# Kernel optimization log

Measured on AMD Instinct MI355X. Metric: run time of the kernel, lower is better.

## Reference

```python
import jax, jax.numpy as jnp
import numpy as np

IN_DIMS = (8, 16, 8)
EMBED = 1024
HEADS = 16
HEAD_DIM = EMBED // HEADS
RANK = 16
CORE_SHAPES = [(1, 8, 8, RANK), (RANK, 16, 16, RANK), (RANK, 8, 8, 1)]


def tt_linear(x, cores, bias):
    """Apply a TT-matrix to x: [N, prod(IN_DIMS)] -> [N, prod(out_dims)].

    Cores G_k: [r_{k-1}, i_k, o_k, r_k], r_0 = r_d = 1. Sequential chain of
    small rank-bounded contractions, faithful to TTLinear.forward.
    """
    N = x.shape[0]
    t = x.reshape(N, 1, 1, -1)  # (N, O_done, r, I_rest)
    for G, i in zip(cores, IN_DIMS):
        rest = t.shape[-1] // i
        t = t.reshape(N, t.shape[1], t.shape[2], i, rest)
        # contract input mode i and left rank r -> output mode q and right rank s
        t = jnp.einsum('norik,riqs->noqsk', t, G)
        t = t.reshape(N, t.shape[1] * t.shape[2], t.shape[3], -1)
    return t.reshape(N, -1) + bias


def setup_inputs() -> dict:
    key = jax.random.key(0)
    ks = iter(jax.random.split(key, 32))
    inp = {"query": jax.random.normal(next(ks), (2, 2048, EMBED), dtype=jnp.float32)}
    for name in ("wq", "wk", "wv", "wo"):
        for ci, shp in enumerate(CORE_SHAPES):
            inp[f"{name}_c{ci}"] = jax.random.normal(next(ks), shp, dtype=jnp.float32) * 0.3
        inp[f"{name}_b"] = jax.random.normal(next(ks), (EMBED,), dtype=jnp.float32) * 0.02
    return inp


def reference(query, wq_c0, wq_c1, wq_c2, wq_b, wk_c0, wk_c1, wk_c2, wk_b,
              wv_c0, wv_c1, wv_c2, wv_b, wo_c0, wo_c1, wo_c2, wo_b):
    B, Lq, _ = query.shape
    flat = query.reshape(-1, EMBED)
    # self-attention: key = value = query
    Q = tt_linear(flat, (wq_c0, wq_c1, wq_c2), wq_b).reshape(B, Lq, HEADS, HEAD_DIM)
    K = tt_linear(flat, (wk_c0, wk_c1, wk_c2), wk_b).reshape(B, Lq, HEADS, HEAD_DIM)
    V = tt_linear(flat, (wv_c0, wv_c1, wv_c2), wv_b).reshape(B, Lq, HEADS, HEAD_DIM)
    Q = Q.transpose(0, 2, 1, 3)  # bhqd
    K = K.transpose(0, 2, 1, 3)
    V = V.transpose(0, 2, 1, 3)
    scale = HEAD_DIM ** -0.5
    scores = jnp.einsum('bhqd,bhkd->bhqk', Q, K) * scale
    attn = jax.nn.softmax(scores, axis=-1)
    ctx = jnp.einsum('bhqk,bhkd->bhqd', attn, V)
    ctx = ctx.transpose(0, 2, 1, 3).reshape(B * Lq, EMBED)
    out = tt_linear(ctx, (wo_c0, wo_c1, wo_c2), wo_b)
    return out.reshape(B, Lq, EMBED)
```

## Files before the change

kernel.cpp:

```cpp
#include <hip/hip_runtime.h>
#include <hip/hip_bf16.h>
#include <stdint.h>

#define LQ 2048
#define NTOK 4096

typedef __attribute__((ext_vector_type(8))) short short8;
typedef __attribute__((ext_vector_type(4))) float f32x4;
typedef __attribute__((ext_vector_type(16))) float f32x16;
typedef __attribute__((ext_vector_type(4))) unsigned short u16x4;

#define MFMA16(a, b, c) __builtin_amdgcn_mfma_f32_16x16x32_bf16((a), (b), (c), 0, 0, 0)
#define MFMA32(a, b, c) __builtin_amdgcn_mfma_f32_32x32x16_bf16((a), (b), (c), 0, 0, 0)

__device__ __forceinline__ unsigned short f2bf(float x) {
    union { __hip_bfloat16 b; unsigned short u; } v;
    v.b = __float2bfloat16(x);
    return v.u;
}
__device__ __forceinline__ float bf2f(unsigned short h) {
    union { uint32_t u; float f; } v; v.u = ((uint32_t)h) << 16; return v.f;
}
__device__ __forceinline__ unsigned int cvtpk_bf16(float lo, float hi_) {
    unsigned int r;
    asm("v_cvt_pk_bf16_f32 %0, %1, %2" : "=v"(r) : "v"(lo), "v"(hi_));
    return r;
}
__device__ __forceinline__ void permswap(unsigned int &a, unsigned int &b) {
    asm("v_permlane32_swap_b32 %0, %1" : "+v"(a), "+v"(b));
}

struct CorePtrs {
    const float* c0[4];
    const float* c1[4];
    const float* c2[4];
};

__global__ __launch_bounds__(256) void build_w_kernel(
    CorePtrs cp, unsigned short* __restrict__ Whi, unsigned short* __restrict__ Wlo)
{
    __shared__ float B1[16 * 16 * 16];
    const int p  = blockIdx.y;
    const int i0 = blockIdx.x >> 3;
    const int q0 = blockIdx.x & 7;
    const int t  = threadIdx.x;
    const float* __restrict__ c0 = cp.c0[p];
    const float* __restrict__ c1 = cp.c1[p];
    const float* __restrict__ c2 = cp.c2[p];

    float g0[16];
#pragma unroll
    for (int s = 0; s < 16; ++s) g0[s] = c0[(i0 * 8 + q0) * 16 + s];

    for (int idx = t; idx < 4096; idx += 256) {
        const int s2 = idx & 15;
        const int q1 = (idx >> 4) & 15;
        const int i1 = idx >> 8;
        float acc = 0.f;
#pragma unroll
        for (int s = 0; s < 16; ++s)
            acc += g0[s] * c1[((s * 16 + i1) * 16 + q1) * 16 + s2];
        B1[idx] = acc;
    }
    __syncthreads();

    const size_t base = (size_t)p * 1024 * 1024;
    for (int idx = t; idx < 16384; idx += 256) {
        const int q2 = idx & 7;
        const int i2 = (idx >> 3) & 7;
        const int q1 = (idx >> 6) & 15;
        const int i1 = idx >> 10;
        float acc = 0.f;
#pragma unroll
        for (int s2 = 0; s2 < 16; ++s2)
            acc += B1[(i1 * 16 + q1) * 16 + s2] * c2[(s2 * 8 + i2) * 8 + q2];
        const int o = q0 * 128 + q1 * 8 + q2;
        const int e = i0 * 128 + i1 * 8 + i2;
        const unsigned short hi = f2bf(acc);
        Whi[base + o * 1024 + e] = hi;
        Wlo[base + o * 1024 + e] = f2bf(acc - bf2f(hi));
    }
}

__global__ __launch_bounds__(256) void convert_x_kernel(
    const float* __restrict__ X, unsigned short* __restrict__ Xhi,
    unsigned short* __restrict__ Xlo, int n4)
{
    const int i = blockIdx.x * 256 + threadIdx.x;
    if (i >= n4) return;
    const float4 v = ((const float4*)X)[i];
    u16x4 hi, lo;
    float vv[4] = {v.x, v.y, v.z, v.w};
#pragma unroll
    for (int j = 0; j < 4; ++j) {
        unsigned short h = f2bf(vv[j]);
        hi[j] = h;
        lo[j] = f2bf(vv[j] - bf2f(h));
    }
    ((u16x4*)Xhi)[i] = hi;
    ((u16x4*)Xlo)[i] = lo;
}

template <bool SPLIT, int OUTMODE>
__global__ __launch_bounds__(256) void gemm_kernel(
    const unsigned short* __restrict__ Xh, const unsigned short* __restrict__ Xl,
    const unsigned short* __restrict__ Wh, const unsigned short* __restrict__ Wl,
    const float* __restrict__ bias, float oscale,
    unsigned short* __restrict__ Yhi, unsigned short* __restrict__ Ylo,
    float* __restrict__ Yf)
{
    __shared__ unsigned short Ah[128 * 32];
    __shared__ unsigned short Bh[128 * 32];
    __shared__ unsigned short Al[SPLIT ? 128 * 32 : 8];
    __shared__ unsigned short Bl[SPLIT ? 128 * 32 : 8];

    const int t = threadIdx.x;
    const int l = t & 63;
    const int w = t >> 6;
    const int wr = (w >> 1) * 64, wc = (w & 1) * 64;
    const int bm = blockIdx.y * 128, bn = blockIdx.x * 128;

    f32x4 acc[4][4];
#pragma unroll
    for (int i = 0; i < 4; ++i)
#pragma unroll
        for (int j = 0; j < 4; ++j) acc[i][j] = (f32x4){0.f, 0.f, 0.f, 0.f};

    const int srow = t >> 1;
    const int sch  = (t & 1) * 2;
    const int ssel = (srow >> 1) & 3;
    const int sd0  = srow * 32 + (((sch)     ^ ssel) << 3);
    const int sd1  = srow * 32 + (((sch + 1) ^ ssel) << 3);
    const size_t xoff = (size_t)(bm + srow) * 1024 + sch * 8;
    const size_t woff = (size_t)(bn + srow) * 1024 + sch * 8;

    const int fsel = ((l & 15) >> 1) & 3;
    const int fpos = ((l >> 4) ^ fsel) << 3;
    const int fra  = (wr + (l & 15)) * 32 + fpos;
    const int frb  = (wc + (l & 15)) * 32 + fpos;

    short8 pXh0, pXh1, pWh0, pWh1, pXl0, pXl1, pWl0, pWl1;
    pXh0 = *(const short8*)&Xh[xoff];     pXh1 = *(const short8*)&Xh[xoff + 8];
    pWh0 = *(const short8*)&Wh[woff];     pWh1 = *(const short8*)&Wh[woff + 8];
    if constexpr (SPLIT) {
        pXl0 = *(const short8*)&Xl[xoff]; pXl1 = *(const short8*)&Xl[xoff + 8];
        pWl0 = *(const short8*)&Wl[woff]; pWl1 = *(const short8*)&Wl[woff + 8];
    }

    for (int e0 = 0; e0 < 1024; e0 += 32) {
        __syncthreads();
        *(short8*)&Ah[sd0] = pXh0; *(short8*)&Ah[sd1] = pXh1;
        *(short8*)&Bh[sd0] = pWh0; *(short8*)&Bh[sd1] = pWh1;
        if constexpr (SPLIT) {
            *(short8*)&Al[sd0] = pXl0; *(short8*)&Al[sd1] = pXl1;
            *(short8*)&Bl[sd0] = pWl0; *(short8*)&Bl[sd1] = pWl1;
        }
        __syncthreads();

        if (e0 + 32 < 1024) {
            const size_t xo = xoff + e0 + 32, wo = woff + e0 + 32;
            pXh0 = *(const short8*)&Xh[xo];     pXh1 = *(const short8*)&Xh[xo + 8];
            pWh0 = *(const short8*)&Wh[wo];     pWh1 = *(const short8*)&Wh[wo + 8];
            if constexpr (SPLIT) {
                pXl0 = *(const short8*)&Xl[xo]; pXl1 = *(const short8*)&Xl[xo + 8];
                pWl0 = *(const short8*)&Wl[wo]; pWl1 = *(const short8*)&Wl[wo + 8];
            }
        }

        short8 af[4], bfv[4], afl[4], bfl[4];
#pragma unroll
        for (int rb = 0; rb < 4; ++rb) {
            af[rb]  = *(const short8*)&Ah[fra + rb * 512];
            bfv[rb] = *(const short8*)&Bh[frb + rb * 512];
        }
#pragma unroll
        for (int rb = 0; rb < 4; ++rb)
#pragma unroll
            for (int cb = 0; cb < 4; ++cb)
                acc[rb][cb] = MFMA16(af[rb], bfv[cb], acc[rb][cb]);
        if constexpr (SPLIT) {
#pragma unroll
            for (int rb = 0; rb < 4; ++rb) afl[rb] = *(const short8*)&Al[fra + rb * 512];
#pragma unroll
            for (int rb = 0; rb < 4; ++rb)
#pragma unroll
                for (int cb = 0; cb < 4; ++cb)
                    acc[rb][cb] = MFMA16(afl[rb], bfv[cb], acc[rb][cb]);
#pragma unroll
            for (int rb = 0; rb < 4; ++rb) bfl[rb] = *(const short8*)&Bl[frb + rb * 512];
#pragma unroll
            for (int rb = 0; rb < 4; ++rb)
#pragma unroll
                for (int cb = 0; cb < 4; ++cb)
                    acc[rb][cb] = MFMA16(af[rb], bfl[cb], acc[rb][cb]);
        }
    }

    const int r0 = (l >> 4) * 4;
    const int cc = l & 15;
#pragma unroll
    for (int rb = 0; rb < 4; ++rb)
#pragma unroll
        for (int cb = 0; cb < 4; ++cb) {
            const int col = bn + wc + cb * 16 + cc;
            const float bv = bias[col];
#pragma unroll
            for (int r = 0; r < 4; ++r) {
                const int row = bm + wr + rb * 16 + r0 + r;
                const float v = (acc[rb][cb][r] + bv) * oscale;
                if constexpr (OUTMODE == 0) {
                    const unsigned short hi = f2bf(v);
                    Yhi[(size_t)row * 1024 + col] = hi;
                    Ylo[(size_t)row * 1024 + col] = f2bf(v - bf2f(hi));
                } else if constexpr (OUTMODE == 1) {
                    Yhi[(size_t)row * 1024 + col] = f2bf(v);
                } else {
                    Yf[(size_t)row * 1024 + col] = v;
                }
            }
        }
}

__global__ __launch_bounds__(256) void transpose_kernel(
    const unsigned short* __restrict__ V, unsigned short* __restrict__ VT)
{
    __shared__ unsigned short tile[64][65];
    const int t = threadIdx.x;
    const int c0 = blockIdx.x * 64;
    const int r0 = blockIdx.y * 64;
    {
        const int r = t >> 2;
        const int q = (t & 3) * 16;
        short8 v0 = *(const short8*)&V[(size_t)(r0 + r) * 1024 + c0 + q];
        short8 v1 = *(const short8*)&V[(size_t)(r0 + r) * 1024 + c0 + q + 8];
#pragma unroll
        for (int i = 0; i < 8; ++i) {
            tile[r][q + i]     = (unsigned short)v0[i];
            tile[r][q + 8 + i] = (unsigned short)v1[i];
        }
    }
    __syncthreads();
    {
        const int c = t >> 2;
        const int g = (t & 3) * 16;
        short8 out0, out1;
#pragma unroll
        for (int i = 0; i < 8; ++i) {
            out0[i] = (short)tile[g + i][c];
            out1[i] = (short)tile[g + 8 + i][c];
        }
        *(short8*)&VT[(size_t)(c0 + c) * 4096 + r0 + g]     = out0;
        *(short8*)&VT[(size_t)(c0 + c) * 4096 + r0 + g + 8] = out1;
    }
}

__global__ __launch_bounds__(256) void attn_kernel(
    const unsigned short* __restrict__ Qh, const unsigned short* __restrict__ Ql,
    const unsigned short* __restrict__ Kh_g, const unsigned short* __restrict__ Kl_g,
    const unsigned short* __restrict__ VT, unsigned short* __restrict__ CTX)
{
    __shared__ unsigned short Khs[2][64 * 64];
    __shared__ unsigned short Kls[2][64 * 64];
    __shared__ unsigned short Vts[2][64 * 64];

    const int t = threadIdx.x;
    const int l = t & 63;
    const int w = t >> 6;
    const int qt = blockIdx.x, h = blockIdx.y, b = blockIdx.z;
    const int lq = l & 31;
    const int hi = l >> 5;
    const int tokq = b * LQ + qt * 128 + w * 32;

    short8 qhf[4], qlf[4];
    {
        const size_t qr = (size_t)(tokq + lq) * 1024 + h * 64 + hi * 8;
#pragma unroll
        for (int ds = 0; ds < 4; ++ds) {
            qhf[ds] = *(const short8*)&Qh[qr + ds * 16];
            qlf[ds] = *(const short8*)&Ql[qr + ds * 16];
        }
    }

    f32x16 o0, o1;
#pragma unroll
    for (int i = 0; i < 16; ++i) { o0[i] = 0.f; o1[i] = 0.f; }
    float m = -1e30f, lsum = 0.f;

    const int srow = t >> 2;
    const int sch  = (t & 3) * 2;
    int sdst[2];
#pragma unroll
    for (int it = 0; it < 2; ++it)
        sdst[it] = srow * 64 + (((sch + it) ^ (srow & 7)) << 3);

    short8 pf_kh[2], pf_kl[2], pf_vt[2];
    {
        const int tokk = b * LQ;
#pragma unroll
        for (int it = 0; it < 2; ++it) {
            const size_t gk = (size_t)(tokk + srow) * 1024 + h * 64 + (sch + it) * 8;
            pf_kh[it] = *(const short8*)&Kh_g[gk];
            pf_kl[it] = *(const short8*)&Kl_g[gk];
            pf_vt[it] = *(const short8*)&VT[(size_t)(h * 64 + srow) * 4096 + tokk + (sch + it) * 8];
        }
    }

    const int lq7 = lq & 7;
    int cur = 0;
    for (int kt = 0; kt < 32; ++kt) {
#pragma unroll
        for (int it = 0; it < 2; ++it) {
            *(short8*)&Khs[cur][sdst[it]] = pf_kh[it];
            *(short8*)&Kls[cur][sdst[it]] = pf_kl[it];
            *(short8*)&Vts[cur][sdst[it]] = pf_vt[it];
        }
        if (kt < 31) {
            const int tokk = b * LQ + (kt + 1) * 64;
#pragma unroll
            for (int it = 0; it < 2; ++it) {
                const size_t gk = (size_t)(tokk + srow) * 1024 + h * 64 + (sch + it) * 8;
                pf_kh[it] = *(const short8*)&Kh_g[gk];
                pf_kl[it] = *(const short8*)&Kl_g[gk];
                pf_vt[it] = *(const short8*)&VT[(size_t)(h * 64 + srow) * 4096 + tokk + (sch + it) * 8];
            }
        }
        __syncthreads();

        f32x16 s0, s1;
#pragma unroll
        for (int i = 0; i < 16; ++i) { s0[i] = 0.f; s1[i] = 0.f; }
#pragma unroll
        for (int ds = 0; ds < 4; ++ds) {
            const int slot = (((2 * ds + hi) ^ lq7) << 3);
            const int off = lq * 64 + slot;
            short8 kh0 = *(const short8*)&Khs[cur][off];
            short8 kh1 = *(const short8*)&Khs[cur][off + 2048];
            short8 kl0 = *(const short8*)&Kls[cur][off];
            short8 kl1 = *(const short8*)&Kls[cur][off + 2048];
            s0 = MFMA32(kh0, qhf[ds], s0);
            s1 = MFMA32(kh1, qhf[ds], s1);
            s0 = MFMA32(kl0, qhf[ds], s0);
            s1 = MFMA32(kl1, qhf[ds], s1);
            s0 = MFMA32(kh0, qlf[ds], s0);
            s1 = MFMA32(kh1, qlf[ds], s1);
        }

        float vm = s0[0];
#pragma unroll
        for (int i = 1; i < 16; ++i) vm = fmaxf(vm, s0[i]);
#pragma unroll
        for (int i = 0; i < 16; ++i) vm = fmaxf(vm, s1[i]);
        vm = fmaxf(vm, __shfl_xor(vm, 32));
        const float mg = fmaxf(m, vm);
        if (__any(mg > m + 8.f)) {
            const float mu = (mg > m + 8.f) ? mg : m;
            const float alpha = exp2f(m - mu);
            lsum *= alpha;
            o0 *= alpha;
            o1 *= alpha;
            m = mu;
        }
        float ps = 0.f;
#pragma unroll
        for (int i = 0; i < 16; ++i) { s0[i] = exp2f(s0[i] - m); ps += s0[i]; }
#pragma unroll
        for (int i = 0; i < 16; ++i) { s1[i] = exp2f(s1[i] - m); ps += s1[i]; }
        lsum += ps;

        unsigned int pw[4][4];
        {
            unsigned int a, bb;
            a = cvtpk_bf16(s0[0], s0[1]); bb = cvtpk_bf16(s0[4], s0[5]);
            permswap(a, bb); pw[0][0] = a; pw[0][2] = bb;
            a = cvtpk_bf16(s0[2], s0[3]); bb = cvtpk_bf16(s0[6], s0[7]);
            permswap(a, bb); pw[0][1] = a; pw[0][3] = bb;
            a = cvtpk_bf16(s0[8], s0[9]); bb = cvtpk_bf16(s0[12], s0[13]);
            permswap(a, bb); pw[1][0] = a; pw[1][2] = bb;
            a = cvtpk_bf16(s0[10], s0[11]); bb = cvtpk_bf16(s0[14], s0[15]);
            permswap(a, bb); pw[1][1] = a; pw[1][3] = bb;
            a = cvtpk_bf16(s1[0], s1[1]); bb = cvtpk_bf16(s1[4], s1[5]);
            permswap(a, bb); pw[2][0] = a; pw[2][2] = bb;
            a = cvtpk_bf16(s1[2], s1[3]); bb = cvtpk_bf16(s1[6], s1[7]);
            permswap(a, bb); pw[2][1] = a; pw[2][3] = bb;
            a = cvtpk_bf16(s1[8], s1[9]); bb = cvtpk_bf16(s1[12], s1[13]);
            permswap(a, bb); pw[3][0] = a; pw[3][2] = bb;
            a = cvtpk_bf16(s1[10], s1[11]); bb = cvtpk_bf16(s1[14], s1[15]);
            permswap(a, bb); pw[3][1] = a; pw[3][3] = bb;
        }

#pragma unroll
        for (int ks = 0; ks < 4; ++ks) {
            union { unsigned int u[4]; short8 v; } pa;
            pa.u[0] = pw[ks][0]; pa.u[1] = pw[ks][1];
            pa.u[2] = pw[ks][2]; pa.u[3] = pw[ks][3];
            const int slot = (((2 * ks + hi) ^ lq7) << 3);
            short8 v0 = *(const short8*)&Vts[cur][lq * 64 + slot];
            short8 v1 = *(const short8*)&Vts[cur][(32 + lq) * 64 + slot];
            o0 = MFMA32(v0, pa.v, o0);
            o1 = MFMA32(v1, pa.v, o1);
        }
        cur ^= 1;
    }

    lsum += __shfl_xor(lsum, 32);
    const float inv = 1.f / lsum;
    const size_t orow = (size_t)(tokq + lq) * 1024 + h * 64 + hi * 4;
#pragma unroll
    for (int g = 0; g < 4; ++g) {
        u16x4 pack0, pack1;
#pragma unroll
        for (int j = 0; j < 4; ++j) {
            pack0[j] = f2bf(o0[4 * g + j] * inv);
            pack1[j] = f2bf(o1[4 * g + j] * inv);
        }
        *(u16x4*)&CTX[orow + 8 * g]      = pack0;
        *(u16x4*)&CTX[orow + 32 + 8 * g] = pack1;
    }
}

extern "C" void kernel_launch(void* const* d_in, const int* in_sizes, int n_in,
                              void* d_out, int out_size, void* d_ws, size_t ws_size,
                              hipStream_t stream)
{
    (void)in_sizes; (void)n_in; (void)out_size; (void)ws_size;
    const float* query = (const float*)d_in[0];
    char* base = (char*)d_ws;
    const size_t MB = 1 << 20;
    unsigned short* Whi = (unsigned short*)(base + 0 * MB);
    unsigned short* Wlo = (unsigned short*)(base + 8 * MB);
    unsigned short* Xhi = (unsigned short*)(base + 16 * MB);
    unsigned short* Xlo = (unsigned short*)(base + 24 * MB);
    unsigned short* Qhi = (unsigned short*)(base + 32 * MB);
    unsigned short* Qlo = (unsigned short*)(base + 40 * MB);
    unsigned short* Khi = (unsigned short*)(base + 48 * MB);
    unsigned short* Klo = (unsigned short*)(base + 56 * MB);
    unsigned short* Vh  = (unsigned short*)(base + 64 * MB);
    unsigned short* VTp = (unsigned short*)(base + 72 * MB);
    unsigned short* CTX = (unsigned short*)(base + 16 * MB);

    CorePtrs cp;
    for (int p = 0; p < 4; ++p) {
        cp.c0[p] = (const float*)d_in[1 + 4 * p];
        cp.c1[p] = (const float*)d_in[2 + 4 * p];
        cp.c2[p] = (const float*)d_in[3 + 4 * p];
    }
    const size_t WSZ = (size_t)1024 * 1024;
    const float QSCALE = 0.125f * 1.44269504088896340736f;

    build_w_kernel<<<dim3(64, 4), 256, 0, stream>>>(cp, Whi, Wlo);
    convert_x_kernel<<<4096, 256, 0, stream>>>(query, Xhi, Xlo, 1048576);

    gemm_kernel<true, 0><<<dim3(8, 32), 256, 0, stream>>>(
        Xhi, Xlo, Whi + 0 * WSZ, Wlo + 0 * WSZ, (const float*)d_in[4], QSCALE,
        Qhi, Qlo, nullptr);
    gemm_kernel<true, 0><<<dim3(8, 32), 256, 0, stream>>>(
        Xhi, Xlo, Whi + 1 * WSZ, Wlo + 1 * WSZ, (const float*)d_in[8], 1.0f,
        Khi, Klo, nullptr);
    gemm_kernel<false, 1><<<dim3(8, 32), 256, 0, stream>>>(
        Xhi, nullptr, Whi + 2 * WSZ, nullptr, (const float*)d_in[12], 1.0f,
        Vh, nullptr, nullptr);

    transpose_kernel<<<dim3(16, 64), 256, 0, stream>>>(Vh, VTp);

    attn_kernel<<<dim3(16, 16, 2), 256, 0, stream>>>(Qhi, Qlo, Khi, Klo, VTp, CTX);

    gemm_kernel<false, 2><<<dim3(8, 32), 256, 0, stream>>>(
        CTX, nullptr, Whi + 3 * WSZ, nullptr, (const float*)d_in[16], 1.0f,
        nullptr, nullptr, (float*)d_out);
}
```

Measured before the change: 325.8 us.

## Fuse QKV projections into one GEMM launch and tune attention inner loop

Merges the three Q/K/V projection GEMMs into a single launch that selects its output buffer, bias and scale from the column block, so the three projections can run concurrently. The attention kernel gains raised wave priority around MFMA sections, a raw v_exp_f32 in place of exp2f, precomputed LDS offsets and incrementing prefetch pointers. The V projection now also uses the hi/lo split path, adding extra MFMA work for V. The fast exp may lose a little accuracy compared with exp2f.

Result: faster. 294.8 us (-9.5%).

```diff
diff --git a/kernel.cpp b/kernel.cpp
--- a/kernel.cpp
+++ b/kernel.cpp
@@ -29,11 +29,23 @@
 __device__ __forceinline__ void permswap(unsigned int &a, unsigned int &b) {
     asm("v_permlane32_swap_b32 %0, %1" : "+v"(a), "+v"(b));
 }
+__device__ __forceinline__ float fast_exp2(float x) {
+    float r;
+    asm("v_exp_f32 %0, %1" : "=v"(r) : "v"(x));
+    return r;
+}
 
 struct CorePtrs {
     const float* c0[4];
     const float* c1[4];
     const float* c2[4];
+};
+
+struct QkvOut {
+    unsigned short* hi[3];
+    unsigned short* lo[2];
+    const float* bias[3];
+    float osc[3];
 };
 
 __global__ __launch_bounds__(256) void build_w_kernel(
@@ -101,18 +113,15 @@
     ((u16x4*)Xlo)[i] = lo;
 }
 
-template <bool SPLIT, int OUTMODE>
-__global__ __launch_bounds__(256) void gemm_kernel(
+__global__ __launch_bounds__(256) void gemm_qkv_kernel(
     const unsigned short* __restrict__ Xh, const unsigned short* __restrict__ Xl,
     const unsigned short* __restrict__ Wh, const unsigned short* __restrict__ Wl,
-    const float* __restrict__ bias, float oscale,
-    unsigned short* __restrict__ Yhi, unsigned short* __restrict__ Ylo,
-    float* __restrict__ Yf)
+    QkvOut op)
 {
     __shared__ unsigned short Ah[128 * 32];
     __shared__ unsigned short Bh[128 * 32];
-    __shared__ unsigned short Al[SPLIT ? 128 * 32 : 8];
-    __shared__ unsigned short Bl[SPLIT ? 128 * 32 : 8];
+    __shared__ unsigned short Al[128 * 32];
+    __shared__ unsigned short Bl[128 * 32];
 
     const int t = threadIdx.x;
     const int l = t & 63;
@@ -142,29 +151,23 @@
     short8 pXh0, pXh1, pWh0, pWh1, pXl0, pXl1, pWl0, pWl1;
     pXh0 = *(const short8*)&Xh[xoff];     pXh1 = *(const short8*)&Xh[xoff + 8];
     pWh0 = *(const short8*)&Wh[woff];     pWh1 = *(const short8*)&Wh[woff + 8];
-    if constexpr (SPLIT) {
-        pXl0 = *(const short8*)&Xl[xoff]; pXl1 = *(const short8*)&Xl[xoff + 8];
-        pWl0 = *(const short8*)&Wl[woff]; pWl1 = *(const short8*)&Wl[woff + 8];
-    }
+    pXl0 = *(const short8*)&Xl[xoff];     pXl1 = *(const short8*)&Xl[xoff + 8];
+    pWl0 = *(const short8*)&Wl[woff];     pWl1 = *(const short8*)&Wl[woff + 8];
 
     for (int e0 = 0; e0 < 1024; e0 += 32) {
         __syncthreads();
         *(short8*)&Ah[sd0] = pXh0; *(short8*)&Ah[sd1] = pXh1;
         *(short8*)&Bh[sd0] = pWh0; *(short8*)&Bh[sd1] = pWh1;
-        if constexpr (SPLIT) {
-            *(short8*)&Al[sd0] = pXl0; *(short8*)&Al[sd1] = pXl1;
-            *(short8*)&Bl[sd0] = pWl0; *(short8*)&Bl[sd1] = pWl1;
-        }
+        *(short8*)&Al[sd0] = pXl0; *(short8*)&Al[sd1] = pXl1;
+        *(short8*)&Bl[sd0] = pWl0; *(short8*)&Bl[sd1] = pWl1;
         __syncthreads();
 
         if (e0 + 32 < 1024) {
             const size_t xo = xoff + e0 + 32, wo = woff + e0 + 32;
             pXh0 = *(const short8*)&Xh[xo];     pXh1 = *(const short8*)&Xh[xo + 8];
             pWh0 = *(const short8*)&Wh[wo];     pWh1 = *(const short8*)&Wh[wo + 8];
-            if constexpr (SPLIT) {
-                pXl0 = *(const short8*)&Xl[xo]; pXl1 = *(const short8*)&Xl[xo + 8];
-                pWl0 = *(const short8*)&Wl[wo]; pWl1 = *(const short8*)&Wl[wo + 8];
-            }
+            pXl0 = *(const short8*)&Xl[xo];     pXl1 = *(const short8*)&Xl[xo + 8];
+            pWl0 = *(const short8*)&Wl[wo];     pWl1 = *(const short8*)&Wl[wo + 8];
         }
 
         short8 af[4], bfv[4], afl[4], bfl[4];
@@ -178,22 +181,110 @@
 #pragma unroll
             for (int cb = 0; cb < 4; ++cb)
                 acc[rb][cb] = MFMA16(af[rb], bfv[cb], acc[rb][cb]);
-        if constexpr (SPLIT) {
-#pragma unroll
-            for (int rb = 0; rb < 4; ++rb) afl[rb] = *(const short8*)&Al[fra + rb * 512];
-#pragma unroll
-            for (int rb = 0; rb < 4; ++rb)
-#pragma unroll
-                for (int cb = 0; cb < 4; ++cb)
-                    acc[rb][cb] = MFMA16(afl[rb], bfv[cb], acc[rb][cb]);
-#pragma unroll
-            for (int rb = 0; rb < 4; ++rb) bfl[rb] = *(const short8*)&Bl[frb + rb * 512];
-#pragma unroll
-            for (int rb = 0; rb < 4; ++rb)
-#pragma unroll
-                for (int cb = 0; cb < 4; ++cb)
-                    acc[rb][cb] = MFMA16(af[rb], bfl[cb], acc[rb][cb]);
-        }
+#pragma unroll
+        for (int rb = 0; rb < 4; ++rb) afl[rb] = *(const short8*)&Al[fra + rb * 512];
+#pragma unroll
+        for (int rb = 0; rb < 4; ++rb)
+#pragma unroll
+            for (int cb = 0; cb < 4; ++cb)
+                acc[rb][cb] = MFMA16(afl[rb], bfv[cb], acc[rb][cb]);
+#pragma unroll
+        for (int rb = 0; rb < 4; ++rb) bfl[rb] = *(const short8*)&Bl[frb + rb * 512];
+#pragma unroll
+        for (int rb = 0; rb < 4; ++rb)
+#pragma unroll
+            for (int cb = 0; cb < 4; ++cb)
+                acc[rb][cb] = MFMA16(af[rb], bfl[cb], acc[rb][cb]);
+    }
+
+    const int p = bn >> 10;
+    unsigned short* __restrict__ yh = op.hi[p];
+    unsigned short* __restrict__ yl = (p < 2) ? op.lo[p] : nullptr;
+    const float* __restrict__ bp = op.bias[p];
+    const float osc = op.osc[p];
+    const int bnl = bn & 1023;
+
+    const int r0 = (l >> 4) * 4;
+    const int cc = l & 15;
+#pragma unroll
+    for (int rb = 0; rb < 4; ++rb)
+#pragma unroll
+        for (int cb = 0; cb < 4; ++cb) {
+            const int col = bnl + wc + cb * 16 + cc;
+            const float bv = bp[col];
+#pragma unroll
+            for (int r = 0; r < 4; ++r) {
+                const int row = bm + wr + rb * 16 + r0 + r;
+                const float v = (acc[rb][cb][r] + bv) * osc;
+                const unsigned short hi = f2bf(v);
+                yh[(size_t)row * 1024 + col] = hi;
+                if (p < 2)
+                    yl[(size_t)row * 1024 + col] = f2bf(v - bf2f(hi));
+            }
+        }
+}
+
+__global__ __launch_bounds__(256) void gemm_out_kernel(
+    const unsigned short* __restrict__ Xh,
+    const unsigned short* __restrict__ Wh,
+    const float* __restrict__ bias,
+    float* __restrict__ Yf)
+{
+    __shared__ unsigned short Ah[128 * 32];
+    __shared__ unsigned short Bh[128 * 32];
+
+    const int t = threadIdx.x;
+    const int l = t & 63;
+    const int w = t >> 6;
+    const int wr = (w >> 1) * 64, wc = (w & 1) * 64;
+    const int bm = blockIdx.y * 128, bn = blockIdx.x * 128;
+
+    f32x4 acc[4][4];
+#pragma unroll
+    for (int i = 0; i < 4; ++i)
+#pragma unroll
+        for (int j = 0; j < 4; ++j) acc[i][j] = (f32x4){0.f, 0.f, 0.f, 0.f};
+
+    const int srow = t >> 1;
+    const int sch  = (t & 1) * 2;
+    const int ssel = (srow >> 1) & 3;
+    const int sd0  = srow * 32 + (((sch)     ^ ssel) << 3);
+    const int sd1  = srow * 32 + (((sch + 1) ^ ssel) << 3);
+    const size_t xoff = (size_t)(bm + srow) * 1024 + sch * 8;
+    const size_t woff = (size_t)(bn + srow) * 1024 + sch * 8;
+
+    const int fsel = ((l & 15) >> 1) & 3;
+    const int fpos = ((l >> 4) ^ fsel) << 3;
+    const int fra  = (wr + (l & 15)) * 32 + fpos;
+    const int frb  = (wc + (l & 15)) * 32 + fpos;
+
+    short8 pXh0, pXh1, pWh0, pWh1;
+    pXh0 = *(const short8*)&Xh[xoff]; pXh1 = *(const short8*)&Xh[xoff + 8];
+    pWh0 = *(const short8*)&Wh[woff]; pWh1 = *(const short8*)&Wh[woff + 8];
+
+    for (int e0 = 0; e0 < 1024; e0 += 32) {
+        __syncthreads();
+        *(short8*)&Ah[sd0] = pXh0; *(short8*)&Ah[sd1] = pXh1;
+        *(short8*)&Bh[sd0] = pWh0; *(short8*)&Bh[sd1] = pWh1;
+        __syncthreads();
+
+        if (e0 + 32 < 1024) {
+            const size_t xo = xoff + e0 + 32, wo = woff + e0 + 32;
+            pXh0 = *(const short8*)&Xh[xo]; pXh1 = *(const short8*)&Xh[xo + 8];
+            pWh0 = *(const short8*)&Wh[wo]; pWh1 = *(const short8*)&Wh[wo + 8];
+        }
+
+        short8 af[4], bfv[4];
+#pragma unroll
+        for (int rb = 0; rb < 4; ++rb) {
+            af[rb]  = *(const short8*)&Ah[fra + rb * 512];
+            bfv[rb] = *(const short8*)&Bh[frb + rb * 512];
+        }
+#pragma unroll
+        for (int rb = 0; rb < 4; ++rb)
+#pragma unroll
+            for (int cb = 0; cb < 4; ++cb)
+                acc[rb][cb] = MFMA16(af[rb], bfv[cb], acc[rb][cb]);
     }
 
     const int r0 = (l >> 4) * 4;
@@ -207,16 +298,7 @@
 #pragma unroll
             for (int r = 0; r < 4; ++r) {
                 const int row = bm + wr + rb * 16 + r0 + r;
-                const float v = (acc[rb][cb][r] + bv) * oscale;
-                if constexpr (OUTMODE == 0) {
-                    const unsigned short hi = f2bf(v);
-                    Yhi[(size_t)row * 1024 + col] = hi;
-                    Ylo[(size_t)row * 1024 + col] = f2bf(v - bf2f(hi));
-                } else if constexpr (OUTMODE == 1) {
-                    Yhi[(size_t)row * 1024 + col] = f2bf(v);
-                } else {
-                    Yf[(size_t)row * 1024 + col] = v;
-                }
+                Yf[(size_t)row * 1024 + col] = acc[rb][cb][r] + bv;
             }
         }
 }
@@ -293,19 +375,23 @@
     for (int it = 0; it < 2; ++it)
         sdst[it] = srow * 64 + (((sch + it) ^ (srow & 7)) << 3);
 
+    const unsigned short* pkh = Kh_g + (size_t)(b * LQ + srow) * 1024 + h * 64 + sch * 8;
+    const unsigned short* pkl = Kl_g + (size_t)(b * LQ + srow) * 1024 + h * 64 + sch * 8;
+    const unsigned short* pvt = VT + (size_t)(h * 64 + srow) * 4096 + b * LQ + sch * 8;
+
     short8 pf_kh[2], pf_kl[2], pf_vt[2];
-    {
-        const int tokk = b * LQ;
-#pragma unroll
-        for (int it = 0; it < 2; ++it) {
-            const size_t gk = (size_t)(tokk + srow) * 1024 + h * 64 + (sch + it) * 8;
-            pf_kh[it] = *(const short8*)&Kh_g[gk];
-            pf_kl[it] = *(const short8*)&Kl_g[gk];
-            pf_vt[it] = *(const short8*)&VT[(size_t)(h * 64 + srow) * 4096 + tokk + (sch + it) * 8];
-        }
-    }
+    pf_kh[0] = *(const short8*)pkh;       pf_kh[1] = *(const short8*)(pkh + 8);
+    pf_kl[0] = *(const short8*)pkl;       pf_kl[1] = *(const short8*)(pkl + 8);
+    pf_vt[0] = *(const short8*)pvt;       pf_vt[1] = *(const short8*)(pvt + 8);
 
     const int lq7 = lq & 7;
+    int qkoff[4], pvslot[4];
+#pragma unroll
+    for (int i = 0; i < 4; ++i) {
+        qkoff[i]  = lq * 64 + (((2 * i + hi) ^ lq7) << 3);
+        pvslot[i] = (((2 * i + hi) ^ lq7) << 3);
+    }
+
     int cur = 0;
     for (int kt = 0; kt < 32; ++kt) {
 #pragma unroll
@@ -315,24 +401,20 @@
             *(short8*)&Vts[cur][sdst[it]] = pf_vt[it];
         }
         if (kt < 31) {
-            const int tokk = b * LQ + (kt + 1) * 64;
-#pragma unroll
-            for (int it = 0; it < 2; ++it) {
-                const size_t gk = (size_t)(tokk + srow) * 1024 + h * 64 + (sch + it) * 8;
-                pf_kh[it] = *(const short8*)&Kh_g[gk];
-                pf_kl[it] = *(const short8*)&Kl_g[gk];
-                pf_vt[it] = *(const short8*)&VT[(size_t)(h * 64 + srow) * 4096 + tokk + (sch + it) * 8];
-            }
+            pkh += 64 * 1024; pkl += 64 * 1024; pvt += 64;
+            pf_kh[0] = *(const short8*)pkh;  pf_kh[1] = *(const short8*)(pkh + 8);
+            pf_kl[0] = *(const short8*)pkl;  pf_kl[1] = *(const short8*)(pkl + 8);
+            pf_vt[0] = *(const short8*)pvt;  pf_vt[1] = *(const short8*)(pvt + 8);
         }
         __syncthreads();
 
         f32x16 s0, s1;
 #pragma unroll
         for (int i = 0; i < 16; ++i) { s0[i] = 0.f; s1[i] = 0.f; }
+        __builtin_amdgcn_s_setprio(1);
 #pragma unroll
         for (int ds = 0; ds < 4; ++ds) {
-            const int slot = (((2 * ds + hi) ^ lq7) << 3);
-            const int off = lq * 64 + slot;
+            const int off = qkoff[ds];
             short8 kh0 = *(const short8*)&Khs[cur][off];
             short8 kh1 = *(const short8*)&Khs[cur][off + 2048];
             short8 kl0 = *(const short8*)&Kls[cur][off];
@@ -344,17 +426,20 @@
             s0 = MFMA32(kh0, qlf[ds], s0);
             s1 = MFMA32(kh1, qlf[ds], s1);
         }
-
-        float vm = s0[0];
-#pragma unroll
-        for (int i = 1; i < 16; ++i) vm = fmaxf(vm, s0[i]);
-#pragma unroll
-        for (int i = 0; i < 16; ++i) vm = fmaxf(vm, s1[i]);
+        __builtin_amdgcn_s_setprio(0);
+
+        float vm = fmaxf(fmaxf(s0[0], s0[1]), s0[2]);
+#pragma unroll
+        for (int i = 3; i < 15; i += 2) vm = fmaxf(fmaxf(s0[i], s0[i + 1]), vm);
+        vm = fmaxf(fmaxf(s0[15], s1[0]), vm);
+#pragma unroll
+        for (int i = 1; i < 15; i += 2) vm = fmaxf(fmaxf(s1[i], s1[i + 1]), vm);
+        vm = fmaxf(s1[15], vm);
         vm = fmaxf(vm, __shfl_xor(vm, 32));
         const float mg = fmaxf(m, vm);
         if (__any(mg > m + 8.f)) {
             const float mu = (mg > m + 8.f) ? mg : m;
-            const float alpha = exp2f(m - mu);
+            const float alpha = fast_exp2(m - mu);
             lsum *= alpha;
             o0 *= alpha;
             o1 *= alpha;
@@ -362,9 +447,9 @@
         }
         float ps = 0.f;
 #pragma unroll
-        for (int i = 0; i < 16; ++i) { s0[i] = exp2f(s0[i] - m); ps += s0[i]; }
-#pragma unroll
-        for (int i = 0; i < 16; ++i) { s1[i] = exp2f(s1[i] - m); ps += s1[i]; }
+        for (int i = 0; i < 16; ++i) { s0[i] = fast_exp2(s0[i] - m); ps += s0[i]; }
+#pragma unroll
+        for (int i = 0; i < 16; ++i) { s1[i] = fast_exp2(s1[i] - m); ps += s1[i]; }
         lsum += ps;
 
         unsigned int pw[4][4];
@@ -388,17 +473,19 @@
             permswap(a, bb); pw[3][1] = a; pw[3][3] = bb;
         }
 
+        __builtin_amdgcn_s_setprio(1);
 #pragma unroll
         for (int ks = 0; ks < 4; ++ks) {
             union { unsigned int u[4]; short8 v; } pa;
             pa.u[0] = pw[ks][0]; pa.u[1] = pw[ks][1];
             pa.u[2] = pw[ks][2]; pa.u[3] = pw[ks][3];
-            const int slot = (((2 * ks + hi) ^ lq7) << 3);
+            const int slot = pvslot[ks];
             short8 v0 = *(const short8*)&Vts[cur][lq * 64 + slot];
             short8 v1 = *(const short8*)&Vts[cur][(32 + lq) * 64 + slot];
             o0 = MFMA32(v0, pa.v, o0);
             o1 = MFMA32(v1, pa.v, o1);
         }
+        __builtin_amdgcn_s_setprio(0);
         cur ^= 1;
     }
 
@@ -450,21 +537,20 @@
     build_w_kernel<<<dim3(64, 4), 256, 0, stream>>>(cp, Whi, Wlo);
     convert_x_kernel<<<4096, 256, 0, stream>>>(query, Xhi, Xlo, 1048576);
 
-    gemm_kernel<true, 0><<<dim3(8, 32), 256, 0, stream>>>(
-        Xhi, Xlo, Whi + 0 * WSZ, Wlo + 0 * WSZ, (const float*)d_in[4], QSCALE,
-        Qhi, Qlo, nullptr);
-    gemm_kernel<true, 0><<<dim3(8, 32), 256, 0, stream>>>(
-        Xhi, Xlo, Whi + 1 * WSZ, Wlo + 1 * WSZ, (const float*)d_in[8], 1.0f,
-        Khi, Klo, nullptr);
-    gemm_kernel<false, 1><<<dim3(8, 32), 256, 0, stream>>>(
-        Xhi, nullptr, Whi + 2 * WSZ, nullptr, (const float*)d_in[12], 1.0f,
-        Vh, nullptr, nullptr);
+    QkvOut op;
+    op.hi[0] = Qhi; op.hi[1] = Khi; op.hi[2] = Vh;
+    op.lo[0] = Qlo; op.lo[1] = Klo;
+    op.bias[0] = (const float*)d_in[4];
+    op.bias[1] = (const float*)d_in[8];
+    op.bias[2] = (const float*)d_in[12];
+    op.osc[0] = QSCALE; op.osc[1] = 1.0f; op.osc[2] = 1.0f;
+
+    gemm_qkv_kernel<<<dim3(24, 32), 256, 0, stream>>>(Xhi, Xlo, Whi, Wlo, op);
 
     transpose_kernel<<<dim3(16, 64), 256, 0, stream>>>(Vh, VTp);
 
     attn_kernel<<<dim3(16, 16, 2), 256, 0, stream>>>(Qhi, Qlo, Khi, Klo, VTp, CTX);
 
-    gemm_kernel<false, 2><<<dim3(8, 32), 256, 0, stream>>>(
-        CTX, nullptr, Whi + 3 * WSZ, nullptr, (const float*)d_in[16], 1.0f,
-        nullptr, nullptr, (float*)d_out);
-}
+    gemm_out_kernel<<<dim3(8, 32), 256, 0, stream>>>(
+        CTX, Whi + 3 * WSZ, (const float*)d_in[16], (float*)d_out);
+}
```
